# Performance work log

Hardware: AMD Instinct MI355X
Metric: run time of the kernel (lower is better)

Reference implementation:

```python
import jax, jax.numpy as jnp
import numpy as np

N_QUBITS = 12
N_LAYERS = 8
BATCH = 1024
DIM = 2 ** N_QUBITS


def _apply_rx(state, theta, wire):
    # state: (B, 2**n) complex64; theta: scalar or (B,)
    B = state.shape[0]
    A, C = 2 ** wire, 2 ** (N_QUBITS - wire - 1)
    s = state.reshape(B, A, 2, C)
    half = theta * 0.5
    c = jnp.reshape(jnp.cos(half), (-1, 1, 1))
    sn = jnp.reshape(jnp.sin(half), (-1, 1, 1))
    s0, s1 = s[:, :, 0], s[:, :, 1]
    out = jnp.stack([c * s0 - 1j * sn * s1, c * s1 - 1j * sn * s0], axis=2)
    return out.reshape(B, DIM)


def _apply_rz(state, theta, wire):
    B = state.shape[0]
    A, C = 2 ** wire, 2 ** (N_QUBITS - wire - 1)
    s = state.reshape(B, A, 2, C)
    half = theta * 0.5
    ph0 = jnp.reshape(jnp.cos(half) - 1j * jnp.sin(half), (-1, 1, 1))  # e^{-i t/2}
    out = jnp.stack([ph0 * s[:, :, 0], jnp.conj(ph0) * s[:, :, 1]], axis=2)
    return out.reshape(B, DIM)


def _apply_cnot(state, control):
    # CNOT on wires (control, control+1)
    B = state.shape[0]
    A, C = 2 ** control, 2 ** (N_QUBITS - control - 2)
    s = state.reshape(B, A, 2, 2, C)
    s1 = s[:, :, 1][:, :, ::-1]  # control=1 -> flip target bit
    out = jnp.stack([s[:, :, 0], s1], axis=2)
    return out.reshape(B, DIM)


def _layer(state, p):
    # one variational layer: CNOT ladder then RX/RZ per qubit; p: (2*n,)
    for i in range(N_QUBITS - 1):
        state = _apply_cnot(state, i)
    for i in range(N_QUBITS):
        state = _apply_rx(state, p[2 * i], i)
        state = _apply_rz(state, p[2 * i + 1], i)
    return state


def _pauliz_expvals(state):
    B = state.shape[0]
    probs = state.real ** 2 + state.imag ** 2  # (B, 2**n)
    zs = []
    for w in range(N_QUBITS):
        A, C = 2 ** w, 2 ** (N_QUBITS - w - 1)
        p = probs.reshape(B, A, 2, C)
        zs.append((p[:, :, 0] - p[:, :, 1]).sum(axis=(1, 2)))
    return jnp.stack(zs, axis=1)  # (B, n_qubits)


def setup_inputs() -> dict:
    key = jax.random.key(0)
    k1, k2, k3 = jax.random.split(key, 3)
    x = jax.random.uniform(k1, (BATCH, N_QUBITS), dtype=jnp.float32)
    qnn_params = jax.random.normal(k2, (N_LAYERS, 2 * N_QUBITS), dtype=jnp.float32)
    linear_weights = jax.random.normal(k3, (N_QUBITS, N_QUBITS), dtype=jnp.float32)
    return {"x": x, "qnn_params": qnn_params, "linear_weights": linear_weights}


def reference(x, qnn_params, linear_weights):
    B = x.shape[0]
    # |0...0> initial state, batched
    state = jnp.zeros((B, DIM), dtype=jnp.complex64).at[:, 0].set(1.0)
    # data encoding: RX(pi * x_i) per wire (batched angles)
    for i in range(N_QUBITS):
        state = _apply_rx(state, x[:, i] * jnp.pi, i)
    # variational layers
    state, _ = jax.lax.scan(lambda s, p: (_layer(s, p), None), state, qnn_params)
    z = _pauliz_expvals(state)  # (B, n_qubits)
    y = jax.nn.relu(z @ linear_weights)
    return jnp.sum(y, axis=-1)  # (B,)
```

## Files before the change

kernel.cpp:

```cpp
#include <hip/hip_runtime.h>

#define NQ 12
#define NLAYERS 8
#define BATCH 1024

typedef float v2f __attribute__((ext_vector_type(2)));


constexpr int hbit(int m){ int h=0; while(m>>(h+1)) ++h; return 1<<h; }

__device__ __forceinline__ v2f vsplat(float s){ v2f v; v.x=s; v.y=s; return v; }
__device__ __forceinline__ v2f vswap(v2f v){ return __builtin_shufflevector(v, v, 1, 0); }
template<int S> __device__ __forceinline__ v2f msw(v2f v){ if constexpr (S) return vswap(v); else return v; }
__device__ __forceinline__ v2f vfma(v2f a, v2f b, v2f c){ return __builtin_elementwise_fma(a,b,c); }

template<int S>
__device__ __forceinline__ void rx_upd(v2f& ro, v2f& io, v2f r, v2f i, v2f pr, v2f pi,
                                       v2f hc2, v2f hs2, v2f ns2){
    ro = vfma(hc2, r, hs2*msw<S>(pi));
    io = vfma(hc2, i, ns2*msw<S>(pr));
}

__device__ __forceinline__ v2f bperm2(int addr, v2f v){
    v2f r;
    r.x = __int_as_float(__builtin_amdgcn_ds_bpermute(addr, __float_as_int(v.x)));
    r.y = __int_as_float(__builtin_amdgcn_ds_bpermute(addr, __float_as_int(v.y)));
    return r;
}

#if __has_builtin(__builtin_amdgcn_permlane32_swap) && __has_builtin(__builtin_amdgcn_permlane16_swap)
#define HAVE_PLSWAP 1
#else
#define HAVE_PLSWAP 0
#endif

#if HAVE_PLSWAP
__device__ __forceinline__ void xp32(float& pr, float& pi, float r, float i){
    auto c1 = __builtin_amdgcn_permlane32_swap(__float_as_uint(r), __float_as_uint(i), false, false);
    auto c2 = __builtin_amdgcn_permlane32_swap(c1[1], c1[0], false, false);
    pr = __uint_as_float(c2[0]);
    pi = __uint_as_float(c2[1]);
}
__device__ __forceinline__ void xp16(float& pr, float& pi, float r, float i){
    auto c1 = __builtin_amdgcn_permlane16_swap(__float_as_uint(r), __float_as_uint(i), false, false);
    auto c2 = __builtin_amdgcn_permlane16_swap(c1[1], c1[0], false, false);
    pr = __uint_as_float(c2[0]);
    pi = __uint_as_float(c2[1]);
}
#endif

template<int CTRL>
__device__ __forceinline__ float dpp1(float v){
    int i = __float_as_int(v);
    return __int_as_float(__builtin_amdgcn_update_dpp(i, i, CTRL, 0xF, 0xF, true));
}
template<int LM>
__device__ __forceinline__ float dppx(float v){
    static_assert(LM >= 1 && LM <= 15, "dpp xor range");
    constexpr int h = (LM >> 2) & 3;
    float r = v;
    if constexpr (h == 1 || h == 2) r = dpp1<0x141>(r);
    if constexpr (h == 3 || h == 2) r = dpp1<0x140>(r);
    constexpr int st = (h==1)?7 : (h==2)?8 : (h==3)?15 : 0;
    constexpr int q = (LM ^ st) & 3;
    if constexpr (q == 1) r = dpp1<0xB1>(r);
    if constexpr (q == 2) r = dpp1<0x4E>(r);
    if constexpr (q == 3) r = dpp1<0x1B>(r);
    return r;
}

template<int JM>
__device__ __forceinline__ void rx_local(v2f (&re2)[16], v2f (&im2)[16], v2f hc2, v2f hs2, v2f ns2){
    if constexpr (JM == 1){
        #pragma unroll
        for (int t=0;t<16;++t){
            v2f r=re2[t], i=im2[t];
            rx_upd<1>(re2[t], im2[t], r, i, r, i, hc2, hs2, ns2);
        }
    } else {
        constexpr int m = JM>>1, HB = hbit(m), S = JM&1;
        #pragma unroll
        for (int t=0;t<16;++t){
            if (t & HB) continue;
            const int t2 = t ^ m;
            v2f ru=re2[t], iu=im2[t], rv=re2[t2], iv=im2[t2];
            rx_upd<S>(re2[t],  im2[t],  ru, iu, rv, iv, hc2, hs2, ns2);
            rx_upd<S>(re2[t2], im2[t2], rv, iv, ru, iu, hc2, hs2, ns2);
        }
    }
}

template<int W>
__device__ __forceinline__ void rx_canon(v2f (&re2)[16], v2f (&im2)[16], float hc, float hs, int lane){
    const v2f hc2 = vsplat(hc), hs2 = vsplat(hs), ns2 = vsplat(-hs);
    if constexpr (W >= 1 && W <= 2){
#if HAVE_PLSWAP
        #pragma unroll
        for (int t=0;t<16;++t){
            v2f r=re2[t], i=im2[t];
            float prx,pix,pry,piy;
            if constexpr (W==1){ xp32(prx,pix,r.x,i.x); xp32(pry,piy,r.y,i.y); }
            else               { xp16(prx,pix,r.x,i.x); xp16(pry,piy,r.y,i.y); }
            v2f pr, pi;
            pr.x=prx; pr.y=pry; pi.x=pix; pi.y=piy;
            rx_upd<0>(re2[t], im2[t], r, i, pr, pi, hc2, hs2, ns2);
        }
#else
        const int addr = ((lane ^ (1<<(6-W))) & 63) << 2;
        #pragma unroll
        for (int t=0;t<16;++t){
            v2f r=re2[t], i=im2[t];
            v2f pi = bperm2(addr, i);
            v2f pr = bperm2(addr, r);
            rx_upd<0>(re2[t], im2[t], r, i, pr, pi, hc2, hs2, ns2);
        }
#endif
    } else if constexpr (W >= 3 && W <= 6){
        constexpr int LM = 1<<(6-W);
        #pragma unroll
        for (int t=0;t<16;++t){
            v2f r=re2[t], i=im2[t];
            v2f pr, pi;
            float a0=dppx<LM>(r.x), a1=dppx<LM>(r.y);
            float b0=dppx<LM>(i.x), b1=dppx<LM>(i.y);
            pr.x=a0; pr.y=a1; pi.x=b0; pi.y=b1;
            rx_upd<0>(re2[t], im2[t], r, i, pr, pi, hc2, hs2, ns2);
        }
    } else {
        rx_local<(1<<(11-W))>(re2, im2, hc2, hs2, ns2);
    }
}

__device__ __forceinline__ void exch_write(const v2f (&re2)[16], const v2f (&im2)[16],
                                           int lane, int wv, float4* lds4){
    float4* wr = lds4 + (wv*16)*64 + lane;
    #pragma unroll
    for (int u=0;u<8;++u){
        float4 fr; fr.x=re2[2*u].x; fr.y=re2[2*u].y; fr.z=re2[2*u+1].x; fr.w=re2[2*u+1].y;
        float4 fi; fi.x=im2[2*u].x; fi.y=im2[2*u].y; fi.z=im2[2*u+1].x; fi.w=im2[2*u+1].y;
        wr[u*64]     = fr;
        wr[(8+u)*64] = fi;
    }
}

__device__ __forceinline__ void perm_rx0(v2f (&re2)[16], v2f (&im2)[16],
                                         float hc, float hs, int lane, int wv,
                                         const float4* lds4){
    const v2f hc2 = vsplat(hc), hs2 = vsplat(hs), ns2 = vsplat(-hs);
    const int sl = ((lane ^ (lane>>1)) & 63) ^ (wv<<5);
    const int rb = (lane & 1) << 2;
    const float4* rdS = lds4 + (wv*16)*64 + sl;
    const float4* rdP = lds4 + ((wv^1)*16)*64 + (sl^32);
    #pragma unroll
    for (int u=0;u<8;++u){
        const int row = (u ^ (u>>1)) ^ rb;
        float4 Fr = rdS[row*64], Fi = rdS[(row+8)*64];
        float4 Gr = rdP[row*64], Gi = rdP[(row+8)*64];
        v2f ar,ai,br,bi, pr,pi,qr,qi;
        if ((u & 1) == 0){
            ar.x=Fr.x; ar.y=Fr.y;  br.x=Fr.w; br.y=Fr.z;
            ai.x=Fi.x; ai.y=Fi.y;  bi.x=Fi.w; bi.y=Fi.z;
            pr.x=Gr.x; pr.y=Gr.y;  qr.x=Gr.w; qr.y=Gr.z;
            pi.x=Gi.x; pi.y=Gi.y;  qi.x=Gi.w; qi.y=Gi.z;
        } else {
            ar.x=Fr.z; ar.y=Fr.w;  br.x=Fr.y; br.y=Fr.x;
            ai.x=Fi.z; ai.y=Fi.w;  bi.x=Fi.y; bi.y=Fi.x;
            pr.x=Gr.z; pr.y=Gr.w;  qr.x=Gr.y; qr.y=Gr.x;
            pi.x=Gi.z; pi.y=Gi.w;  qi.x=Gi.y; qi.y=Gi.x;
        }
        rx_upd<0>(re2[2*u],   im2[2*u],   ar, ai, pr, pi, hc2, hs2, ns2);
        rx_upd<0>(re2[2*u+1], im2[2*u+1], br, bi, qr, qi, hc2, hs2, ns2);
    }
}

__device__ __forceinline__ void init_rx0(v2f (&re2)[16], v2f (&im2)[16],
                                         float hc, float hs, int lane, int wv, float4* lds4){
    const v2f hc2 = vsplat(hc), hs2 = vsplat(hs), ns2 = vsplat(-hs);
    exch_write(re2, im2, lane, wv, lds4);
    __syncthreads();
    const float4* rd = lds4 + ((wv^1)*16)*64 + lane;
    #pragma unroll
    for (int u=0;u<8;++u){
        float4 Fr = rd[u*64], Fi = rd[(u+8)*64];
        v2f prl,pil,prh,pih;
        prl.x=Fr.x; prl.y=Fr.y; prh.x=Fr.z; prh.y=Fr.w;
        pil.x=Fi.x; pil.y=Fi.y; pih.x=Fi.z; pih.y=Fi.w;
        rx_upd<0>(re2[2*u],   im2[2*u],   re2[2*u],   im2[2*u],   prl, pil, hc2, hs2, ns2);
        rx_upd<0>(re2[2*u+1], im2[2*u+1], re2[2*u+1], im2[2*u+1], prh, pih, hc2, hs2, ns2);
    }
    __syncthreads();
}

template<int W>
__device__ __forceinline__ void gates_w(v2f (&re2)[16], v2f (&im2)[16],
                                        const float2* __restrict__ tb, int lane){
    const float2 t = tb[W];
    rx_canon<W>(re2, im2, t.x, t.y, lane);
    if constexpr (W+1 < NQ) gates_w<W+1>(re2, im2, tb, lane);
}

template<int W>
__device__ __forceinline__ void init_w(v2f (&re2)[16], v2f (&im2)[16],
                                       const float* __restrict__ xb, int lane){
    float hs, hc;
    __sincosf(xb[W]*1.5707963267948966f, &hs, &hc);
    rx_canon<W>(re2, im2, hc, hs, lane);
    if constexpr (W+1 < NQ) init_w<W+1>(re2, im2, xb, lane);
}

__global__ void prep_kernel(const float* __restrict__ P, float* __restrict__ ws){
    const int i = threadIdx.x;
    float2* tRX = (float2*)ws;
    float*  tTH = ws + 192;
    float4* tJ  = (float4*)(ws + 256);
    if (i < 96){
        const int l = i/12, w = i%12;
        float2 v; __sincosf(P[l*24 + 2*w]*0.5f, &v.y, &v.x);
        tRX[i] = v;
    }
    if (i < 64){
        const int l = i>>3, w = i&7;
        tTH[i] = (w < 7) ? P[l*24 + 2*w + 1]*0.5f : 0.f;
    }
    {
        const int l = i>>4, t = i&15;
        float br[2], bi[2];
        #pragma unroll
        for (int k=0;k<2;++k){
            const int j = 2*t + k;
            float beta = 0.f;
            #pragma unroll
            for (int w=7; w<12; ++w){
                const float th = P[l*24 + 2*w + 1]*0.5f;
                beta += ((j >> (11-w)) & 1) ? th : -th;
            }
            __sincosf(beta, &bi[k], &br[k]);
        }
        float4 v; v.x=br[0]; v.y=br[1]; v.z=bi[0]; v.w=bi[1];
        tJ[i] = v;
    }
}

__global__ __launch_bounds__(128, 2) void qnn_kernel(const float* __restrict__ x,
                                                     const float* __restrict__ ws,
                                                     const float* __restrict__ Wm,
                                                     float* __restrict__ out)
{
    __shared__ float4 lds4[2*16*64];
    const int lane = threadIdx.x & 63;
    const int wv   = threadIdx.x >> 6;
    const int b    = blockIdx.x;

    const float2* tRX = (const float2*)ws;
    const float*  tTH = ws + 192;
    const float4* tJ  = (const float4*)(ws + 256);

    v2f re2[16], im2[16];
    #pragma unroll
    for (int t=0;t<16;++t){ re2[t] = vsplat(0.f); im2[t] = vsplat(0.f); }
    if (threadIdx.x == 0) re2[0].x = 1.0f;

    const float* xb = x + b*NQ;
    init_w<1>(re2, im2, xb, lane);
    {
        float hs0, hc0;
        __sincosf(xb[0]*1.5707963267948966f, &hs0, &hc0);
        init_rx0(re2, im2, hc0, hs0, lane, wv, lds4);
    }

    #pragma unroll 1
    for (int l = 0; l < NLAYERS; ++l){
        const float2* tb = tRX + l*12;
        const float2 t0 = tb[0];
        exch_write(re2, im2, lane, wv, lds4);
        __syncthreads();
        perm_rx0(re2, im2, t0.x, t0.y, lane, wv, lds4);
        gates_w<1>(re2, im2, tb, lane);

        const float* th = tTH + l*8;
        float alpha = wv ? th[0] : -th[0];
        #pragma unroll
        for (int w=1; w<=6; ++w)
            alpha += ((lane >> (6-w)) & 1) ? th[w] : -th[w];
        float sa, ca;
        __sincosf(alpha, &sa, &ca);
        const v2f vca = vsplat(ca), vsa = vsplat(sa), vna = vsplat(-sa);
        const float4* tj = tJ + l*16;
        #pragma unroll
        for (int t=0;t<16;++t){
            const float4 J = tj[t];
            v2f jr; jr.x=J.x; jr.y=J.y;
            v2f ji; ji.x=J.z; ji.y=J.w;
            const v2f cr = vfma(vca, jr, vna*ji);
            const v2f ci = vfma(vca, ji, vsa*jr);
            const v2f nci = -ci;
            const v2f r = re2[t], m = im2[t];
            re2[t] = vfma(r, cr, m*nci);
            im2[t] = vfma(m, cr, r*ci);
        }
        __syncthreads();
    }

    v2f S = vsplat(0.f), S7 = vsplat(0.f), S8 = vsplat(0.f), S9 = vsplat(0.f), S10 = vsplat(0.f);
    #pragma unroll
    for (int t=0;t<16;++t){
        v2f p2 = __builtin_elementwise_fma(re2[t], re2[t], im2[t]*im2[t]);
        S += p2;
        S7  += (t&8)? -p2 : p2;
        S8  += (t&4)? -p2 : p2;
        S9  += (t&2)? -p2 : p2;
        S10 += (t&1)? -p2 : p2;
    }
    const float s0 = S.x + S.y;

    float z[12];
    z[0] = wv ? -s0 : s0;
    #pragma unroll
    for (int w=1; w<=6; ++w) z[w] = ((lane >> (6-w)) & 1) ? -s0 : s0;
    z[7]  = S7.x + S7.y;
    z[8]  = S8.x + S8.y;
    z[9]  = S9.x + S9.y;
    z[10] = S10.x + S10.y;
    z[11] = S.x - S.y;

    #pragma unroll
    for (int m=1; m<64; m<<=1){
        #pragma unroll
        for (int w=0; w<12; ++w) z[w] += __shfl_xor(z[w], m, 64);
    }

    float* sh = (float*)lds4;
    if (lane == 0){
        #pragma unroll
        for (int w=0; w<12; ++w) sh[wv*12 + w] = z[w];
    }
    __syncthreads();
    if (wv == 0){
        float t = 0.f;
        if (lane < 12){
            #pragma unroll
            for (int w=0; w<12; ++w){
                float zz = sh[w] + sh[12+w];
                t = fmaf(zz, Wm[w*12 + lane], t);
            }
            t = fmaxf(t, 0.f);
        }
        #pragma unroll
        for (int m=1; m<16; m<<=1) t += __shfl_xor(t, m, 64);
        if (lane == 0) out[b] = t;
    }
}

extern "C" void kernel_launch(void* const* d_in, const int* in_sizes, int n_in,
                              void* d_out, int out_size, void* d_ws, size_t ws_size,
                              hipStream_t stream) {
    const float* x  = (const float*)d_in[0];
    const float* P  = (const float*)d_in[1];
    const float* Wm = (const float*)d_in[2];
    float* out = (float*)d_out;
    float* ws  = (float*)d_ws;
    prep_kernel<<<1, 128, 0, stream>>>(P, ws);
    qnn_kernel<<<BATCH, 128, 0, stream>>>(x, ws, Wm, out);
}
```

Before: 71.13 us.

## Process two batch samples per block with interleaved state registers

Each block now simulates two batch elements at once, keeping two full state vectors in registers and interleaving their gate updates, LDS exchanges and reductions. This halves the grid to BATCH/2 blocks, shares barrier and parameter-load costs between two samples, and gives more independent instructions to hide latency. In exchange it doubles register and LDS use per block and drops launch bounds to one block per CU, so occupancy falls and fewer blocks fill the GPU.

```diff
diff --git a/kernel.cpp b/kernel.cpp
--- a/kernel.cpp
+++ b/kernel.cpp
@@ -132,8 +132,8 @@
 }
 
 __device__ __forceinline__ void exch_write(const v2f (&re2)[16], const v2f (&im2)[16],
-                                           int lane, int wv, float4* lds4){
-    float4* wr = lds4 + (wv*16)*64 + lane;
+                                           int lane, int wv, float4* buf){
+    float4* wr = buf + (wv*16)*64 + lane;
     #pragma unroll
     for (int u=0;u<8;++u){
         float4 fr; fr.x=re2[2*u].x; fr.y=re2[2*u].y; fr.z=re2[2*u+1].x; fr.w=re2[2*u+1].y;
@@ -145,12 +145,12 @@
 
 __device__ __forceinline__ void perm_rx0(v2f (&re2)[16], v2f (&im2)[16],
                                          float hc, float hs, int lane, int wv,
-                                         const float4* lds4){
+                                         const float4* buf){
     const v2f hc2 = vsplat(hc), hs2 = vsplat(hs), ns2 = vsplat(-hs);
     const int sl = ((lane ^ (lane>>1)) & 63) ^ (wv<<5);
     const int rb = (lane & 1) << 2;
-    const float4* rdS = lds4 + (wv*16)*64 + sl;
-    const float4* rdP = lds4 + ((wv^1)*16)*64 + (sl^32);
+    const float4* rdS = buf + (wv*16)*64 + sl;
+    const float4* rdP = buf + ((wv^1)*16)*64 + (sl^32);
     #pragma unroll
     for (int u=0;u<8;++u){
         const int row = (u ^ (u>>1)) ^ rb;
@@ -173,12 +173,11 @@
     }
 }
 
-__device__ __forceinline__ void init_rx0(v2f (&re2)[16], v2f (&im2)[16],
-                                         float hc, float hs, int lane, int wv, float4* lds4){
+__device__ __forceinline__ void init_rx0_read(v2f (&re2)[16], v2f (&im2)[16],
+                                              float hc, float hs, int lane, int wv,
+                                              const float4* buf){
     const v2f hc2 = vsplat(hc), hs2 = vsplat(hs), ns2 = vsplat(-hs);
-    exch_write(re2, im2, lane, wv, lds4);
-    __syncthreads();
-    const float4* rd = lds4 + ((wv^1)*16)*64 + lane;
+    const float4* rd = buf + ((wv^1)*16)*64 + lane;
     #pragma unroll
     for (int u=0;u<8;++u){
         float4 Fr = rd[u*64], Fi = rd[(u+8)*64];
@@ -188,24 +187,29 @@
         rx_upd<0>(re2[2*u],   im2[2*u],   re2[2*u],   im2[2*u],   prl, pil, hc2, hs2, ns2);
         rx_upd<0>(re2[2*u+1], im2[2*u+1], re2[2*u+1], im2[2*u+1], prh, pih, hc2, hs2, ns2);
     }
-    __syncthreads();
 }
 
 template<int W>
-__device__ __forceinline__ void gates_w(v2f (&re2)[16], v2f (&im2)[16],
+__device__ __forceinline__ void gatesAB(v2f (&Ar)[16], v2f (&Ai)[16],
+                                        v2f (&Br)[16], v2f (&Bi)[16],
                                         const float2* __restrict__ tb, int lane){
     const float2 t = tb[W];
-    rx_canon<W>(re2, im2, t.x, t.y, lane);
-    if constexpr (W+1 < NQ) gates_w<W+1>(re2, im2, tb, lane);
+    rx_canon<W>(Ar, Ai, t.x, t.y, lane);
+    rx_canon<W>(Br, Bi, t.x, t.y, lane);
+    if constexpr (W+1 < NQ) gatesAB<W+1>(Ar, Ai, Br, Bi, tb, lane);
 }
 
 template<int W>
-__device__ __forceinline__ void init_w(v2f (&re2)[16], v2f (&im2)[16],
-                                       const float* __restrict__ xb, int lane){
-    float hs, hc;
-    __sincosf(xb[W]*1.5707963267948966f, &hs, &hc);
-    rx_canon<W>(re2, im2, hc, hs, lane);
-    if constexpr (W+1 < NQ) init_w<W+1>(re2, im2, xb, lane);
+__device__ __forceinline__ void init_wAB(v2f (&Ar)[16], v2f (&Ai)[16],
+                                         v2f (&Br)[16], v2f (&Bi)[16],
+                                         const float* __restrict__ xb0,
+                                         const float* __restrict__ xb1, int lane){
+    float hs0, hc0, hs1, hc1;
+    __sincosf(xb0[W]*1.5707963267948966f, &hs0, &hc0);
+    __sincosf(xb1[W]*1.5707963267948966f, &hs1, &hc1);
+    rx_canon<W>(Ar, Ai, hc0, hs0, lane);
+    rx_canon<W>(Br, Bi, hc1, hs1, lane);
+    if constexpr (W+1 < NQ) init_wAB<W+1>(Ar, Ai, Br, Bi, xb0, xb1, lane);
 }
 
 __global__ void prep_kernel(const float* __restrict__ P, float* __restrict__ ws){
@@ -241,41 +245,56 @@
     }
 }
 
-__global__ __launch_bounds__(128, 2) void qnn_kernel(const float* __restrict__ x,
+__global__ __launch_bounds__(128, 1) void qnn_kernel(const float* __restrict__ x,
                                                      const float* __restrict__ ws,
                                                      const float* __restrict__ Wm,
                                                      float* __restrict__ out)
 {
-    __shared__ float4 lds4[2*16*64];
+    __shared__ float4 lds4[4096];
+    float4* bufA = lds4;
+    float4* bufB = lds4 + 2048;
     const int lane = threadIdx.x & 63;
     const int wv   = threadIdx.x >> 6;
-    const int b    = blockIdx.x;
+    const int b0   = blockIdx.x*2;
+    const int b1   = b0 + 1;
 
     const float2* tRX = (const float2*)ws;
     const float*  tTH = ws + 192;
     const float4* tJ  = (const float4*)(ws + 256);
 
-    v2f re2[16], im2[16];
-    #pragma unroll
-    for (int t=0;t<16;++t){ re2[t] = vsplat(0.f); im2[t] = vsplat(0.f); }
-    if (threadIdx.x == 0) re2[0].x = 1.0f;
-
-    const float* xb = x + b*NQ;
-    init_w<1>(re2, im2, xb, lane);
+    v2f Ar[16], Ai[16], Br[16], Bi[16];
+    #pragma unroll
+    for (int t=0;t<16;++t){
+        Ar[t]=vsplat(0.f); Ai[t]=vsplat(0.f);
+        Br[t]=vsplat(0.f); Bi[t]=vsplat(0.f);
+    }
+    if (threadIdx.x == 0){ Ar[0].x = 1.0f; Br[0].x = 1.0f; }
+
+    const float* xb0 = x + b0*NQ;
+    const float* xb1 = x + b1*NQ;
+    init_wAB<1>(Ar, Ai, Br, Bi, xb0, xb1, lane);
     {
-        float hs0, hc0;
-        __sincosf(xb[0]*1.5707963267948966f, &hs0, &hc0);
-        init_rx0(re2, im2, hc0, hs0, lane, wv, lds4);
+        float hsA, hcA, hsB, hcB;
+        __sincosf(xb0[0]*1.5707963267948966f, &hsA, &hcA);
+        __sincosf(xb1[0]*1.5707963267948966f, &hsB, &hcB);
+        exch_write(Ar, Ai, lane, wv, bufA);
+        exch_write(Br, Bi, lane, wv, bufB);
+        __syncthreads();
+        init_rx0_read(Ar, Ai, hcA, hsA, lane, wv, bufA);
+        init_rx0_read(Br, Bi, hcB, hsB, lane, wv, bufB);
+        __syncthreads();
     }
 
     #pragma unroll 1
     for (int l = 0; l < NLAYERS; ++l){
         const float2* tb = tRX + l*12;
         const float2 t0 = tb[0];
-        exch_write(re2, im2, lane, wv, lds4);
+        exch_write(Ar, Ai, lane, wv, bufA);
+        exch_write(Br, Bi, lane, wv, bufB);
         __syncthreads();
-        perm_rx0(re2, im2, t0.x, t0.y, lane, wv, lds4);
-        gates_w<1>(re2, im2, tb, lane);
+        perm_rx0(Ar, Ai, t0.x, t0.y, lane, wv, bufA);
+        perm_rx0(Br, Bi, t0.x, t0.y, lane, wv, bufB);
+        gatesAB<1>(Ar, Ai, Br, Bi, tb, lane);
 
         const float* th = tTH + l*8;
         float alpha = wv ? th[0] : -th[0];
@@ -291,63 +310,85 @@
             const float4 J = tj[t];
             v2f jr; jr.x=J.x; jr.y=J.y;
             v2f ji; ji.x=J.z; ji.y=J.w;
-            const v2f cr = vfma(vca, jr, vna*ji);
-            const v2f ci = vfma(vca, ji, vsa*jr);
+            const v2f cr  = vfma(vca, jr, vna*ji);
+            const v2f ci  = vfma(vca, ji, vsa*jr);
             const v2f nci = -ci;
-            const v2f r = re2[t], m = im2[t];
-            re2[t] = vfma(r, cr, m*nci);
-            im2[t] = vfma(m, cr, r*ci);
+            v2f r, m;
+            r = Ar[t]; m = Ai[t];
+            Ar[t] = vfma(r, cr, m*nci);
+            Ai[t] = vfma(m, cr, r*ci);
+            r = Br[t]; m = Bi[t];
+            Br[t] = vfma(r, cr, m*nci);
+            Bi[t] = vfma(m, cr, r*ci);
         }
         __syncthreads();
     }
 
-    v2f S = vsplat(0.f), S7 = vsplat(0.f), S8 = vsplat(0.f), S9 = vsplat(0.f), S10 = vsplat(0.f);
+    v2f SA = vsplat(0.f), SA7 = vsplat(0.f), SA8 = vsplat(0.f), SA9 = vsplat(0.f), SA10 = vsplat(0.f);
+    v2f SB = vsplat(0.f), SB7 = vsplat(0.f), SB8 = vsplat(0.f), SB9 = vsplat(0.f), SB10 = vsplat(0.f);
     #pragma unroll
     for (int t=0;t<16;++t){
-        v2f p2 = __builtin_elementwise_fma(re2[t], re2[t], im2[t]*im2[t]);
-        S += p2;
-        S7  += (t&8)? -p2 : p2;
-        S8  += (t&4)? -p2 : p2;
-        S9  += (t&2)? -p2 : p2;
-        S10 += (t&1)? -p2 : p2;
-    }
-    const float s0 = S.x + S.y;
-
-    float z[12];
-    z[0] = wv ? -s0 : s0;
-    #pragma unroll
-    for (int w=1; w<=6; ++w) z[w] = ((lane >> (6-w)) & 1) ? -s0 : s0;
-    z[7]  = S7.x + S7.y;
-    z[8]  = S8.x + S8.y;
-    z[9]  = S9.x + S9.y;
-    z[10] = S10.x + S10.y;
-    z[11] = S.x - S.y;
+        v2f pa = __builtin_elementwise_fma(Ar[t], Ar[t], Ai[t]*Ai[t]);
+        v2f pb = __builtin_elementwise_fma(Br[t], Br[t], Bi[t]*Bi[t]);
+        SA += pa;  SB += pb;
+        SA7  += (t&8)? -pa : pa;   SB7  += (t&8)? -pb : pb;
+        SA8  += (t&4)? -pa : pa;   SB8  += (t&4)? -pb : pb;
+        SA9  += (t&2)? -pa : pa;   SB9  += (t&2)? -pb : pb;
+        SA10 += (t&1)? -pa : pa;   SB10 += (t&1)? -pb : pb;
+    }
+    const float sA0 = SA.x + SA.y;
+    const float sB0 = SB.x + SB.y;
+
+    float zA[12], zB[12];
+    zA[0] = wv ? -sA0 : sA0;  zB[0] = wv ? -sB0 : sB0;
+    #pragma unroll
+    for (int w=1; w<=6; ++w){
+        const bool f = (lane >> (6-w)) & 1;
+        zA[w] = f ? -sA0 : sA0;
+        zB[w] = f ? -sB0 : sB0;
+    }
+    zA[7]  = SA7.x + SA7.y;    zB[7]  = SB7.x + SB7.y;
+    zA[8]  = SA8.x + SA8.y;    zB[8]  = SB8.x + SB8.y;
+    zA[9]  = SA9.x + SA9.y;    zB[9]  = SB9.x + SB9.y;
+    zA[10] = SA10.x + SA10.y;  zB[10] = SB10.x + SB10.y;
+    zA[11] = SA.x - SA.y;      zB[11] = SB.x - SB.y;
 
     #pragma unroll
     for (int m=1; m<64; m<<=1){
         #pragma unroll
-        for (int w=0; w<12; ++w) z[w] += __shfl_xor(z[w], m, 64);
+        for (int w=0; w<12; ++w){
+            zA[w] += __shfl_xor(zA[w], m, 64);
+            zB[w] += __shfl_xor(zB[w], m, 64);
+        }
     }
 
     float* sh = (float*)lds4;
     if (lane == 0){
         #pragma unroll
-        for (int w=0; w<12; ++w) sh[wv*12 + w] = z[w];
+        for (int w=0; w<12; ++w){
+            sh[wv*12 + w]      = zA[w];
+            sh[24 + wv*12 + w] = zB[w];
+        }
     }
     __syncthreads();
     if (wv == 0){
-        float t = 0.f;
+        float tA = 0.f, tB = 0.f;
         if (lane < 12){
             #pragma unroll
             for (int w=0; w<12; ++w){
-                float zz = sh[w] + sh[12+w];
-                t = fmaf(zz, Wm[w*12 + lane], t);
+                const float wm = Wm[w*12 + lane];
+                tA = fmaf(sh[w]      + sh[12+w], wm, tA);
+                tB = fmaf(sh[24+w]   + sh[36+w], wm, tB);
             }
-            t = fmaxf(t, 0.f);
-        }
-        #pragma unroll
-        for (int m=1; m<16; m<<=1) t += __shfl_xor(t, m, 64);
-        if (lane == 0) out[b] = t;
+            tA = fmaxf(tA, 0.f);
+            tB = fmaxf(tB, 0.f);
+        }
+        #pragma unroll
+        for (int m=1; m<16; m<<=1){
+            tA += __shfl_xor(tA, m, 64);
+            tB += __shfl_xor(tB, m, 64);
+        }
+        if (lane == 0){ out[b0] = tA; out[b1] = tB; }
     }
 }
 
@@ -360,5 +401,5 @@
     float* out = (float*)d_out;
     float* ws  = (float*)d_ws;
     prep_kernel<<<1, 128, 0, stream>>>(P, ws);
-    qnn_kernel<<<BATCH, 128, 0, stream>>>(x, ws, Wm, out);
-}
+    qnn_kernel<<<BATCH/2, 128, 0, stream>>>(x, ws, Wm, out);
+}
```

Result: slower. 87.80 us (+23.4%).

## Map each batch state to a single wavefront with in-register permute restore

Applied to the files above, without the earlier changes.

Each 4096-amplitude state is now held by one 64-lane wavefront with 32 complex pairs per lane, instead of being split across two waves in a 128-thread block. The per-layer CNOT-ladder permutation now uses ds_permute on registers rather than an LDS exchange with __syncthreads, and four batch elements share each 256-thread block. This removes block-level barriers and LDS traffic, at the cost of doubling register usage per thread, which may lower occupancy or cause spills. The number of cross-lane permute instructions per layer also rises.

```diff
diff --git a/kernel.cpp b/kernel.cpp
--- a/kernel.cpp
+++ b/kernel.cpp
@@ -19,13 +19,6 @@
                                        v2f hc2, v2f hs2, v2f ns2){
     ro = vfma(hc2, r, hs2*msw<S>(pi));
     io = vfma(hc2, i, ns2*msw<S>(pr));
-}
-
-__device__ __forceinline__ v2f bperm2(int addr, v2f v){
-    v2f r;
-    r.x = __int_as_float(__builtin_amdgcn_ds_bpermute(addr, __float_as_int(v.x)));
-    r.y = __int_as_float(__builtin_amdgcn_ds_bpermute(addr, __float_as_int(v.y)));
-    return r;
 }
 
 #if __has_builtin(__builtin_amdgcn_permlane32_swap) && __has_builtin(__builtin_amdgcn_permlane16_swap)
@@ -48,6 +41,10 @@
     pi = __uint_as_float(c2[1]);
 }
 #endif
+
+__device__ __forceinline__ float bperm1(int addr, float v){
+    return __int_as_float(__builtin_amdgcn_ds_bpermute(addr, __float_as_int(v)));
+}
 
 template<int CTRL>
 __device__ __forceinline__ float dpp1(float v){
@@ -70,17 +67,18 @@
 }
 
 template<int JM>
-__device__ __forceinline__ void rx_local(v2f (&re2)[16], v2f (&im2)[16], v2f hc2, v2f hs2, v2f ns2){
+__device__ __forceinline__ void rx_local32(v2f (&re2)[32], v2f (&im2)[32],
+                                           v2f hc2, v2f hs2, v2f ns2){
     if constexpr (JM == 1){
         #pragma unroll
-        for (int t=0;t<16;++t){
+        for (int t=0;t<32;++t){
             v2f r=re2[t], i=im2[t];
             rx_upd<1>(re2[t], im2[t], r, i, r, i, hc2, hs2, ns2);
         }
     } else {
         constexpr int m = JM>>1, HB = hbit(m), S = JM&1;
         #pragma unroll
-        for (int t=0;t<16;++t){
+        for (int t=0;t<32;++t){
             if (t & HB) continue;
             const int t2 = t ^ m;
             v2f ru=re2[t], iu=im2[t], rv=re2[t2], iv=im2[t2];
@@ -91,34 +89,36 @@
 }
 
 template<int W>
-__device__ __forceinline__ void rx_canon(v2f (&re2)[16], v2f (&im2)[16], float hc, float hs, int lane){
+__device__ __forceinline__ void rx_canon(v2f (&re2)[32], v2f (&im2)[32],
+                                         float hc, float hs, int lane){
     const v2f hc2 = vsplat(hc), hs2 = vsplat(hs), ns2 = vsplat(-hs);
-    if constexpr (W >= 1 && W <= 2){
+    if constexpr (W <= 1){
 #if HAVE_PLSWAP
         #pragma unroll
-        for (int t=0;t<16;++t){
+        for (int t=0;t<32;++t){
             v2f r=re2[t], i=im2[t];
             float prx,pix,pry,piy;
-            if constexpr (W==1){ xp32(prx,pix,r.x,i.x); xp32(pry,piy,r.y,i.y); }
+            if constexpr (W==0){ xp32(prx,pix,r.x,i.x); xp32(pry,piy,r.y,i.y); }
             else               { xp16(prx,pix,r.x,i.x); xp16(pry,piy,r.y,i.y); }
             v2f pr, pi;
             pr.x=prx; pr.y=pry; pi.x=pix; pi.y=piy;
             rx_upd<0>(re2[t], im2[t], r, i, pr, pi, hc2, hs2, ns2);
         }
 #else
-        const int addr = ((lane ^ (1<<(6-W))) & 63) << 2;
-        #pragma unroll
-        for (int t=0;t<16;++t){
+        const int addr = ((lane ^ (32>>W)) & 63) << 2;
+        #pragma unroll
+        for (int t=0;t<32;++t){
             v2f r=re2[t], i=im2[t];
-            v2f pi = bperm2(addr, i);
-            v2f pr = bperm2(addr, r);
+            v2f pr, pi;
+            pr.x = bperm1(addr, r.x); pr.y = bperm1(addr, r.y);
+            pi.x = bperm1(addr, i.x); pi.y = bperm1(addr, i.y);
             rx_upd<0>(re2[t], im2[t], r, i, pr, pi, hc2, hs2, ns2);
         }
 #endif
-    } else if constexpr (W >= 3 && W <= 6){
-        constexpr int LM = 1<<(6-W);
-        #pragma unroll
-        for (int t=0;t<16;++t){
+    } else if constexpr (W <= 5){
+        constexpr int LM = 1<<(5-W);
+        #pragma unroll
+        for (int t=0;t<32;++t){
             v2f r=re2[t], i=im2[t];
             v2f pr, pi;
             float a0=dppx<LM>(r.x), a1=dppx<LM>(r.y);
@@ -127,72 +127,33 @@
             rx_upd<0>(re2[t], im2[t], r, i, pr, pi, hc2, hs2, ns2);
         }
     } else {
-        rx_local<(1<<(11-W))>(re2, im2, hc2, hs2, ns2);
-    }
-}
-
-__device__ __forceinline__ void exch_write(const v2f (&re2)[16], const v2f (&im2)[16],
-                                           int lane, int wv, float4* lds4){
-    float4* wr = lds4 + (wv*16)*64 + lane;
-    #pragma unroll
-    for (int u=0;u<8;++u){
-        float4 fr; fr.x=re2[2*u].x; fr.y=re2[2*u].y; fr.z=re2[2*u+1].x; fr.w=re2[2*u+1].y;
-        float4 fi; fi.x=im2[2*u].x; fi.y=im2[2*u].y; fi.z=im2[2*u+1].x; fi.w=im2[2*u+1].y;
-        wr[u*64]     = fr;
-        wr[(8+u)*64] = fi;
-    }
-}
-
-__device__ __forceinline__ void perm_rx0(v2f (&re2)[16], v2f (&im2)[16],
-                                         float hc, float hs, int lane, int wv,
-                                         const float4* lds4){
-    const v2f hc2 = vsplat(hc), hs2 = vsplat(hs), ns2 = vsplat(-hs);
-    const int sl = ((lane ^ (lane>>1)) & 63) ^ (wv<<5);
-    const int rb = (lane & 1) << 2;
-    const float4* rdS = lds4 + (wv*16)*64 + sl;
-    const float4* rdP = lds4 + ((wv^1)*16)*64 + (sl^32);
-    #pragma unroll
-    for (int u=0;u<8;++u){
-        const int row = (u ^ (u>>1)) ^ rb;
-        float4 Fr = rdS[row*64], Fi = rdS[(row+8)*64];
-        float4 Gr = rdP[row*64], Gi = rdP[(row+8)*64];
-        v2f ar,ai,br,bi, pr,pi,qr,qi;
-        if ((u & 1) == 0){
-            ar.x=Fr.x; ar.y=Fr.y;  br.x=Fr.w; br.y=Fr.z;
-            ai.x=Fi.x; ai.y=Fi.y;  bi.x=Fi.w; bi.y=Fi.z;
-            pr.x=Gr.x; pr.y=Gr.y;  qr.x=Gr.w; qr.y=Gr.z;
-            pi.x=Gi.x; pi.y=Gi.y;  qi.x=Gi.w; qi.y=Gi.z;
-        } else {
-            ar.x=Fr.z; ar.y=Fr.w;  br.x=Fr.y; br.y=Fr.x;
-            ai.x=Fi.z; ai.y=Fi.w;  bi.x=Fi.y; bi.y=Fi.x;
-            pr.x=Gr.z; pr.y=Gr.w;  qr.x=Gr.y; qr.y=Gr.x;
-            pi.x=Gi.z; pi.y=Gi.w;  qi.x=Gi.y; qi.y=Gi.x;
-        }
-        rx_upd<0>(re2[2*u],   im2[2*u],   ar, ai, pr, pi, hc2, hs2, ns2);
-        rx_upd<0>(re2[2*u+1], im2[2*u+1], br, bi, qr, qi, hc2, hs2, ns2);
-    }
-}
-
-__device__ __forceinline__ void init_rx0(v2f (&re2)[16], v2f (&im2)[16],
-                                         float hc, float hs, int lane, int wv, float4* lds4){
-    const v2f hc2 = vsplat(hc), hs2 = vsplat(hs), ns2 = vsplat(-hs);
-    exch_write(re2, im2, lane, wv, lds4);
-    __syncthreads();
-    const float4* rd = lds4 + ((wv^1)*16)*64 + lane;
-    #pragma unroll
-    for (int u=0;u<8;++u){
-        float4 Fr = rd[u*64], Fi = rd[(u+8)*64];
-        v2f prl,pil,prh,pih;
-        prl.x=Fr.x; prl.y=Fr.y; prh.x=Fr.z; prh.y=Fr.w;
-        pil.x=Fi.x; pil.y=Fi.y; pih.x=Fi.z; pih.y=Fi.w;
-        rx_upd<0>(re2[2*u],   im2[2*u],   re2[2*u],   im2[2*u],   prl, pil, hc2, hs2, ns2);
-        rx_upd<0>(re2[2*u+1], im2[2*u+1], re2[2*u+1], im2[2*u+1], prh, pih, hc2, hs2, ns2);
-    }
-    __syncthreads();
+        rx_local32<(1<<(11-W))>(re2, im2, hc2, hs2, ns2);
+    }
+}
+
+template<int J>
+__device__ __forceinline__ float getsc(const v2f (&a)[32]){
+    if constexpr (J & 1) return a[J>>1].y; else return a[J>>1].x;
+}
+
+__device__ __forceinline__ void restore_arr(v2f (&a)[32], int pfx_addr, bool pp){
+    float n[64];
+    #pragma unroll
+    for (int j=0;j<64;++j){
+        const int ja = j ^ (j>>1);
+        const int tA = ja >> 1, tB = tA ^ 16;
+        float sA, sB;
+        if (ja & 1){ sA = a[tA].y; sB = a[tB].y; }
+        else       { sA = a[tA].x; sB = a[tB].x; }
+        const float sel = pp ? sB : sA;
+        n[j] = __int_as_float(__builtin_amdgcn_ds_permute(pfx_addr, __float_as_int(sel)));
+    }
+    #pragma unroll
+    for (int t=0;t<32;++t){ a[t].x = n[2*t]; a[t].y = n[2*t+1]; }
 }
 
 template<int W>
-__device__ __forceinline__ void gates_w(v2f (&re2)[16], v2f (&im2)[16],
+__device__ __forceinline__ void gates_w(v2f (&re2)[32], v2f (&im2)[32],
                                         const float2* __restrict__ tb, int lane){
     const float2 t = tb[W];
     rx_canon<W>(re2, im2, t.x, t.y, lane);
@@ -200,7 +161,7 @@
 }
 
 template<int W>
-__device__ __forceinline__ void init_w(v2f (&re2)[16], v2f (&im2)[16],
+__device__ __forceinline__ void init_w(v2f (&re2)[32], v2f (&im2)[32],
                                        const float* __restrict__ xb, int lane){
     float hs, hc;
     __sincosf(xb[W]*1.5707963267948966f, &hs, &hc);
@@ -220,103 +181,98 @@
     }
     if (i < 64){
         const int l = i>>3, w = i&7;
-        tTH[i] = (w < 7) ? P[l*24 + 2*w + 1]*0.5f : 0.f;
+        tTH[i] = (w < 6) ? P[l*24 + 2*w + 1]*0.5f : 0.f;
     }
     {
-        const int l = i>>4, t = i&15;
+        const int l = i>>5, t = i&31;
         float br[2], bi[2];
         #pragma unroll
         for (int k=0;k<2;++k){
             const int j = 2*t + k;
             float beta = 0.f;
             #pragma unroll
-            for (int w=7; w<12; ++w){
+            for (int w=6; w<12; ++w){
                 const float th = P[l*24 + 2*w + 1]*0.5f;
                 beta += ((j >> (11-w)) & 1) ? th : -th;
             }
             __sincosf(beta, &bi[k], &br[k]);
         }
         float4 v; v.x=br[0]; v.y=br[1]; v.z=bi[0]; v.w=bi[1];
-        tJ[i] = v;
-    }
-}
-
-__global__ __launch_bounds__(128, 2) void qnn_kernel(const float* __restrict__ x,
+        tJ[l*32 + t] = v;
+    }
+}
+
+__global__ __launch_bounds__(256, 1) void qnn_kernel(const float* __restrict__ x,
                                                      const float* __restrict__ ws,
                                                      const float* __restrict__ Wm,
                                                      float* __restrict__ out)
 {
-    __shared__ float4 lds4[2*16*64];
     const int lane = threadIdx.x & 63;
-    const int wv   = threadIdx.x >> 6;
-    const int b    = blockIdx.x;
+    const int wid  = threadIdx.x >> 6;
+    const int b    = blockIdx.x*4 + wid;
 
     const float2* tRX = (const float2*)ws;
     const float*  tTH = ws + 192;
     const float4* tJ  = (const float4*)(ws + 256);
 
-    v2f re2[16], im2[16];
-    #pragma unroll
-    for (int t=0;t<16;++t){ re2[t] = vsplat(0.f); im2[t] = vsplat(0.f); }
-    if (threadIdx.x == 0) re2[0].x = 1.0f;
-
-    const float* xb = x + b*NQ;
-    init_w<1>(re2, im2, xb, lane);
-    {
-        float hs0, hc0;
-        __sincosf(xb[0]*1.5707963267948966f, &hs0, &hc0);
-        init_rx0(re2, im2, hc0, hs0, lane, wv, lds4);
-    }
+    int pf = lane; pf ^= pf>>1; pf ^= pf>>2; pf ^= pf>>4;
+    const int pfx_addr = (pf & 63) << 2;
+    const bool pp = (__popc(lane) & 1) != 0;
+
+    v2f re2[32], im2[32];
+    #pragma unroll
+    for (int t=0;t<32;++t){ re2[t] = vsplat(0.f); im2[t] = vsplat(0.f); }
+    if (lane == 0) re2[0].x = 1.0f;
+
+    init_w<0>(re2, im2, x + b*NQ, lane);
 
     #pragma unroll 1
     for (int l = 0; l < NLAYERS; ++l){
-        const float2* tb = tRX + l*12;
-        const float2 t0 = tb[0];
-        exch_write(re2, im2, lane, wv, lds4);
-        __syncthreads();
-        perm_rx0(re2, im2, t0.x, t0.y, lane, wv, lds4);
-        gates_w<1>(re2, im2, tb, lane);
+        restore_arr(re2, pfx_addr, pp);
+        restore_arr(im2, pfx_addr, pp);
+        gates_w<0>(re2, im2, tRX + l*12, lane);
 
         const float* th = tTH + l*8;
-        float alpha = wv ? th[0] : -th[0];
-        #pragma unroll
-        for (int w=1; w<=6; ++w)
-            alpha += ((lane >> (6-w)) & 1) ? th[w] : -th[w];
+        float alpha = 0.f;
+        #pragma unroll
+        for (int w=0; w<=5; ++w)
+            alpha += ((lane >> (5-w)) & 1) ? th[w] : -th[w];
         float sa, ca;
         __sincosf(alpha, &sa, &ca);
         const v2f vca = vsplat(ca), vsa = vsplat(sa), vna = vsplat(-sa);
-        const float4* tj = tJ + l*16;
-        #pragma unroll
-        for (int t=0;t<16;++t){
+        const float4* tj = tJ + l*32;
+        #pragma unroll
+        for (int t=0;t<32;++t){
             const float4 J = tj[t];
             v2f jr; jr.x=J.x; jr.y=J.y;
             v2f ji; ji.x=J.z; ji.y=J.w;
-            const v2f cr = vfma(vca, jr, vna*ji);
-            const v2f ci = vfma(vca, ji, vsa*jr);
+            const v2f cr  = vfma(vca, jr, vna*ji);
+            const v2f ci  = vfma(vca, ji, vsa*jr);
             const v2f nci = -ci;
             const v2f r = re2[t], m = im2[t];
             re2[t] = vfma(r, cr, m*nci);
             im2[t] = vfma(m, cr, r*ci);
         }
-        __syncthreads();
-    }
-
-    v2f S = vsplat(0.f), S7 = vsplat(0.f), S8 = vsplat(0.f), S9 = vsplat(0.f), S10 = vsplat(0.f);
-    #pragma unroll
-    for (int t=0;t<16;++t){
+    }
+
+    v2f S = vsplat(0.f), S6 = vsplat(0.f), S7 = vsplat(0.f), S8 = vsplat(0.f),
+        S9 = vsplat(0.f), S10 = vsplat(0.f);
+    #pragma unroll
+    for (int t=0;t<32;++t){
         v2f p2 = __builtin_elementwise_fma(re2[t], re2[t], im2[t]*im2[t]);
         S += p2;
-        S7  += (t&8)? -p2 : p2;
-        S8  += (t&4)? -p2 : p2;
-        S9  += (t&2)? -p2 : p2;
-        S10 += (t&1)? -p2 : p2;
+        S6  += (t&16)? -p2 : p2;
+        S7  += (t& 8)? -p2 : p2;
+        S8  += (t& 4)? -p2 : p2;
+        S9  += (t& 2)? -p2 : p2;
+        S10 += (t& 1)? -p2 : p2;
     }
     const float s0 = S.x + S.y;
 
     float z[12];
-    z[0] = wv ? -s0 : s0;
-    #pragma unroll
-    for (int w=1; w<=6; ++w) z[w] = ((lane >> (6-w)) & 1) ? -s0 : s0;
+    #pragma unroll
+    for (int w=0; w<=5; ++w) z[w] = ((lane >> (5-w)) & 1) ? -s0 : s0;
+    z[6]  = S6.x + S6.y;
     z[7]  = S7.x + S7.y;
     z[8]  = S8.x + S8.y;
     z[9]  = S9.x + S9.y;
@@ -329,26 +285,16 @@
         for (int w=0; w<12; ++w) z[w] += __shfl_xor(z[w], m, 64);
     }
 
-    float* sh = (float*)lds4;
-    if (lane == 0){
-        #pragma unroll
-        for (int w=0; w<12; ++w) sh[wv*12 + w] = z[w];
-    }
-    __syncthreads();
-    if (wv == 0){
-        float t = 0.f;
-        if (lane < 12){
-            #pragma unroll
-            for (int w=0; w<12; ++w){
-                float zz = sh[w] + sh[12+w];
-                t = fmaf(zz, Wm[w*12 + lane], t);
-            }
-            t = fmaxf(t, 0.f);
-        }
-        #pragma unroll
-        for (int m=1; m<16; m<<=1) t += __shfl_xor(t, m, 64);
-        if (lane == 0) out[b] = t;
-    }
+    float tacc = 0.f;
+    if (lane < 12){
+        #pragma unroll
+        for (int w=0; w<12; ++w)
+            tacc = fmaf(z[w], Wm[w*12 + lane], tacc);
+        tacc = fmaxf(tacc, 0.f);
+    }
+    #pragma unroll
+    for (int m=1; m<16; m<<=1) tacc += __shfl_xor(tacc, m, 64);
+    if (lane == 0) out[b] = tacc;
 }
 
 extern "C" void kernel_launch(void* const* d_in, const int* in_sizes, int n_in,
@@ -359,6 +305,6 @@
     const float* Wm = (const float*)d_in[2];
     float* out = (float*)d_out;
     float* ws  = (float*)d_ws;
-    prep_kernel<<<1, 128, 0, stream>>>(P, ws);
-    qnn_kernel<<<BATCH, 128, 0, stream>>>(x, ws, Wm, out);
-}
+    prep_kernel<<<1, 256, 0, stream>>>(P, ws);
+    qnn_kernel<<<BATCH/4, 256, 0, stream>>>(x, ws, Wm, out);
+}
```

Result: slower. 97.00 us (+36.4%).
